# Performance work log

Hardware: AMD Instinct MI355X
Metric: run time of the kernel (lower is better)

The kernel has to match this reference:

```python
import jax, jax.numpy as jnp
import numpy as np

N, E = 50000, 500000
D_IN, D_HID, D_OUT = 512, 512, 256


def setup_inputs() -> dict:
    key = jax.random.key(0)
    ks = jax.random.split(key, 8)
    x = jax.random.normal(ks[0], (N, D_IN), dtype=jnp.float32)
    edge_index1 = jax.random.randint(ks[1], (2, E), 0, N, dtype=jnp.int64)
    edge_index2 = jax.random.randint(ks[2], (2, E), 0, N, dtype=jnp.int64)
    s_in = 1.0 / np.sqrt(D_IN)
    s_hid = 1.0 / np.sqrt(D_HID)
    W1l = jax.random.normal(ks[3], (D_HID, D_IN), dtype=jnp.float32) * s_in
    W1r = jax.random.normal(ks[4], (D_HID, D_IN), dtype=jnp.float32) * s_in
    b1 = jnp.zeros((D_HID,), dtype=jnp.float32)
    W2l = jax.random.normal(ks[5], (D_OUT, D_HID), dtype=jnp.float32) * s_hid
    W2r = jax.random.normal(ks[6], (D_OUT, D_HID), dtype=jnp.float32) * s_hid
    b2 = jnp.zeros((D_OUT,), dtype=jnp.float32)
    return {"x": x, "edge_index1": edge_index1, "edge_index2": edge_index2,
            "W1l": W1l, "b1": b1, "W1r": W1r, "W2l": W2l, "b2": b2, "W2r": W2r}


def _sage_conv(x_src, x_dst, edge_index, Wl, b, Wr):
    # PyG SAGEConv (aggr='mean', root_weight=True): lin_l(mean_agg) + lin_r(x_dst)
    src, dst = edge_index[0], edge_index[1]
    n_dst = x_dst.shape[0]
    msgs = x_src[src]                                        # [E, d] gather
    agg = jax.ops.segment_sum(msgs, dst, num_segments=n_dst)  # [n_dst, d]
    deg = jax.ops.segment_sum(jnp.ones((src.shape[0],), x_src.dtype), dst,
                              num_segments=n_dst)
    agg = agg / jnp.maximum(deg, 1.0)[:, None]                # mean
    return agg @ Wl.T + b + x_dst @ Wr.T


def reference(x, edge_index1, edge_index2, W1l, b1, W1r, W2l, b2, W2r):
    # layer 1 (+ relu; dropout is identity in eval mode)
    h = _sage_conv(x, x, edge_index1, W1l, b1, W1r)
    h = jax.nn.relu(h)
    # layer 2
    h = _sage_conv(h, h, edge_index2, W2l, b2, W2r)
    return jax.nn.log_softmax(h, axis=-1)
```

## Files before the change

kernel.cpp:

```cpp
#include <hip/hip_runtime.h>
#include <math.h>

#define DIN  512
#define DHID 512
#define DOUT 256

typedef __attribute__((ext_vector_type(8))) short short8;
typedef __attribute__((ext_vector_type(4))) float f32x4;
typedef __attribute__((ext_vector_type(2))) float floatx2;

__device__ __forceinline__ unsigned short f2bf(float f) {
    unsigned int u = __float_as_uint(f);
    u += 0x7fffu + ((u >> 16) & 1u);
    return (unsigned short)(u >> 16);
}
__device__ __forceinline__ float bflo(unsigned int w) { return __uint_as_float(w << 16); }
__device__ __forceinline__ float bfhi(unsigned int w) { return __uint_as_float(w & 0xffff0000u); }

__device__ __forceinline__ void cvt8(const float* __restrict__ in,
                                     unsigned short* __restrict__ out, int i) {
    const float4* iv = (const float4*)in;
    float4 a = iv[2 * i], b = iv[2 * i + 1];
    uint4 o;
    o.x = (unsigned)f2bf(a.x) | ((unsigned)f2bf(a.y) << 16);
    o.y = (unsigned)f2bf(a.z) | ((unsigned)f2bf(a.w) << 16);
    o.z = (unsigned)f2bf(b.x) | ((unsigned)f2bf(b.y) << 16);
    o.w = (unsigned)f2bf(b.z) | ((unsigned)f2bf(b.w) << 16);
    ((uint4*)out)[i] = o;
}

__global__ void k_f2bf(const float* __restrict__ in, unsigned short* __restrict__ out, int n8) {
    int i = blockIdx.x * blockDim.x + threadIdx.x;
    if (i < n8) cvt8(in, out, i);
}

__global__ void k_wcvt(const float* __restrict__ W1l, const float* __restrict__ W1r,
                       const float* __restrict__ W2l, const float* __restrict__ W2r,
                       unsigned short* __restrict__ w1, unsigned short* __restrict__ w2) {
    int i = blockIdx.x * blockDim.x + threadIdx.x;
    if (i < 32768)        cvt8(W1l, w1, i);
    else if (i < 65536)   cvt8(W1r, w1 + 262144, i - 32768);
    else if (i < 81920)   cvt8(W2l, w2, i - 65536);
    else if (i < 98304)   cvt8(W2r, w2 + 131072, i - 81920);
}

__global__ void k_count2(const int* __restrict__ d1, const int* __restrict__ d2,
                         int* __restrict__ deg1, int* __restrict__ deg2, int E1, int E2) {
    int e = blockIdx.x * blockDim.x + threadIdx.x;
    if (blockIdx.y == 0) { if (e < E1) atomicAdd(&deg1[d1[e]], 1); }
    else                 { if (e < E2) atomicAdd(&deg2[d2[e]], 1); }
}

#define SCAN_B 256
__global__ void k_scan_partial2(const int* __restrict__ deg1, const int* __restrict__ deg2,
                                int* __restrict__ part1, int* __restrict__ part2, int n) {
    __shared__ int s[SCAN_B];
    const int* deg = blockIdx.y ? deg2 : deg1;
    int* part      = blockIdx.y ? part2 : part1;
    int i = blockIdx.x * SCAN_B + threadIdx.x;
    s[threadIdx.x] = (i < n) ? deg[i] : 0;
    __syncthreads();
    for (int off = SCAN_B / 2; off > 0; off >>= 1) {
        if (threadIdx.x < off) s[threadIdx.x] += s[threadIdx.x + off];
        __syncthreads();
    }
    if (threadIdx.x == 0) part[blockIdx.x] = s[0];
}

__global__ void k_scan_part2b(int* __restrict__ part1, int* __restrict__ part2, int nb,
                              int* __restrict__ rowptr1, int* __restrict__ rowptr2, int n) {
    __shared__ int s[SCAN_B];
    int* part   = blockIdx.x ? part2 : part1;
    int* rowptr = blockIdx.x ? rowptr2 : rowptr1;
    int v = (threadIdx.x < nb) ? part[threadIdx.x] : 0;
    s[threadIdx.x] = v;
    __syncthreads();
    for (int off = 1; off < SCAN_B; off <<= 1) {
        int t = (threadIdx.x >= off) ? s[threadIdx.x - off] : 0;
        __syncthreads();
        s[threadIdx.x] += t;
        __syncthreads();
    }
    if (threadIdx.x < nb) part[threadIdx.x] = s[threadIdx.x] - v;
    if (threadIdx.x == SCAN_B - 1) rowptr[n] = s[SCAN_B - 1];
}

__global__ void k_scan_final2(const int* __restrict__ deg1, const int* __restrict__ deg2,
                              const int* __restrict__ part1, const int* __restrict__ part2,
                              int* __restrict__ rowptr1, int* __restrict__ rowptr2,
                              int* __restrict__ cursor1, int* __restrict__ cursor2, int n) {
    __shared__ int s[SCAN_B];
    const int* deg  = blockIdx.y ? deg2 : deg1;
    const int* part = blockIdx.y ? part2 : part1;
    int* rowptr     = blockIdx.y ? rowptr2 : rowptr1;
    int* cursor     = blockIdx.y ? cursor2 : cursor1;
    int i = blockIdx.x * SCAN_B + threadIdx.x;
    int v = (i < n) ? deg[i] : 0;
    s[threadIdx.x] = v;
    __syncthreads();
    for (int off = 1; off < SCAN_B; off <<= 1) {
        int t = (threadIdx.x >= off) ? s[threadIdx.x - off] : 0;
        __syncthreads();
        s[threadIdx.x] += t;
        __syncthreads();
    }
    if (i < n) {
        int ex = part[blockIdx.y ? blockIdx.x : blockIdx.x] + s[threadIdx.x] - v;
        rowptr[i] = ex;
        cursor[i] = ex;
    }
}

__global__ void k_fill2(const int* __restrict__ s1, const int* __restrict__ d1,
                        const int* __restrict__ s2, const int* __restrict__ d2,
                        int* __restrict__ cur1, int* __restrict__ cur2,
                        int* __restrict__ col1, int* __restrict__ col2, int E1, int E2) {
    int e = blockIdx.x * blockDim.x + threadIdx.x;
    if (blockIdx.y == 0) {
        if (e < E1) { int p = atomicAdd(&cur1[d1[e]], 1); col1[p] = s1[e]; }
    } else {
        if (e < E2) { int p = atomicAdd(&cur2[d2[e]], 1); col2[p] = s2[e]; }
    }
}

#define TM 128
#define TN 128
#define TK 32

template <int NCT, int SPLIT>
__global__ __launch_bounds__(256, 3)
void k_gemm_mfma(const unsigned short* __restrict__ A, const unsigned short* __restrict__ W,
                 unsigned char* __restrict__ C8, unsigned short* __restrict__ C16,
                 int M, int K, int NC) {
    __shared__ __align__(16) unsigned short As[TM * TK];
    __shared__ __align__(16) unsigned short Bs[TN * TK];
    const int id = blockIdx.x;
    const int xcd = id & 7;
    const int s = id >> 3;
    const int row0 = ((s / NCT) * 8 + xcd) * TM;
    const int col0 = (s % NCT) * TN;
    if (row0 >= M) return;

    const int t = threadIdx.x;
    const int lane = t & 63;
    const int w = t >> 6;
    const int wr = (w >> 1) * 64;
    const int wc = (w & 1) * 64;
    const int lm = lane & 15;
    const int k8 = (lane >> 4) * 8;

    f32x4 acc[4][4];
#pragma unroll
    for (int i = 0; i < 4; ++i)
#pragma unroll
        for (int j = 0; j < 4; ++j) acc[i][j] = (f32x4){0.f, 0.f, 0.f, 0.f};

    const int ar = t >> 2;
    const int as = (t & 3) * 8;

    for (int k0 = 0; k0 < K; k0 += TK) {
        int r1 = row0 + ar;      if (r1 >= M) r1 = M - 1;
        int r2 = row0 + ar + 64; if (r2 >= M) r2 = M - 1;
        const unsigned short* ga1 = A + (size_t)r1 * K + k0 + as;
        const unsigned short* ga2 = A + (size_t)r2 * K + k0 + as;
        const unsigned short* gb1 = W + (size_t)(col0 + ar) * K + k0 + as;
        const unsigned short* gb2 = W + (size_t)(col0 + ar + 64) * K + k0 + as;
        __builtin_amdgcn_global_load_lds(
            (const __attribute__((address_space(1))) unsigned int*)ga1,
            (__attribute__((address_space(3))) unsigned int*)&As[t * 8], 16, 0, 0);
        __builtin_amdgcn_global_load_lds(
            (const __attribute__((address_space(1))) unsigned int*)ga2,
            (__attribute__((address_space(3))) unsigned int*)&As[(t + 256) * 8], 16, 0, 0);
        __builtin_amdgcn_global_load_lds(
            (const __attribute__((address_space(1))) unsigned int*)gb1,
            (__attribute__((address_space(3))) unsigned int*)&Bs[t * 8], 16, 0, 0);
        __builtin_amdgcn_global_load_lds(
            (const __attribute__((address_space(1))) unsigned int*)gb2,
            (__attribute__((address_space(3))) unsigned int*)&Bs[(t + 256) * 8], 16, 0, 0);
        __syncthreads();

        short8 a[4], b[4];
#pragma unroll
        for (int i = 0; i < 4; ++i)
            a[i] = *(const short8*)&As[(wr + i * 16 + lm) * TK + k8];
#pragma unroll
        for (int j = 0; j < 4; ++j)
            b[j] = *(const short8*)&Bs[(wc + j * 16 + lm) * TK + k8];
#pragma unroll
        for (int i = 0; i < 4; ++i)
#pragma unroll
            for (int j = 0; j < 4; ++j)
                acc[i][j] = __builtin_amdgcn_mfma_f32_16x16x32_bf16(a[i], b[j], acc[i][j], 0, 0, 0);
        __syncthreads();
    }

    const int qr = (lane >> 4) * 4;
    const bool lo_half = SPLIT && (col0 < NC / 2);
    const int cadj = SPLIT ? NC / 2 : 0;
#pragma unroll
    for (int i = 0; i < 4; ++i) {
#pragma unroll
        for (int r = 0; r < 4; ++r) {
            int gr = row0 + wr + i * 16 + qr + r;
            if (gr >= M) continue;
#pragma unroll
            for (int j = 0; j < 4; ++j) {
                int gc = col0 + wc + j * 16 + lm;
                float v = acc[i][j][r];
                if (SPLIT && lo_half) {
                    int p = __builtin_amdgcn_cvt_pk_fp8_f32(v, v, 0, 0);
                    C8[(size_t)gr * (NC / 2) + gc] = (unsigned char)p;
                } else {
                    C16[(size_t)gr * (NC - cadj) + (gc - cadj)] = f2bf(v);
                }
            }
        }
    }
}

__global__ void k_agg_relu(const unsigned char* __restrict__ C8,
                           const unsigned short* __restrict__ C16r,
                           const int* __restrict__ rowptr, const int* __restrict__ col,
                           const float* __restrict__ b1, unsigned short* __restrict__ H, int n) {
    int node = blockIdx.x * (blockDim.x >> 6) + (threadIdx.x >> 6);
    int lane = threadIdx.x & 63;
    if (node >= n) return;
    int beg = rowptr[node], end = rowptr[node + 1];
    float acc[8] = {};
    const uint2* Cv = (const uint2*)C8;
    int e = beg;
    for (; e + 4 <= end; e += 4) {
        int c0 = col[e], c1 = col[e + 1], c2 = col[e + 2], c3 = col[e + 3];
        uint2 v0 = Cv[(size_t)c0 * 64 + lane];
        uint2 v1 = Cv[(size_t)c1 * 64 + lane];
        uint2 v2 = Cv[(size_t)c2 * 64 + lane];
        uint2 v3 = Cv[(size_t)c3 * 64 + lane];
        unsigned int ws[8] = {v0.x, v0.y, v1.x, v1.y, v2.x, v2.y, v3.x, v3.y};
#pragma unroll
        for (int q = 0; q < 8; ++q) {
            floatx2 flo = __builtin_amdgcn_cvt_pk_f32_fp8(ws[q], 0);
            floatx2 fhi = __builtin_amdgcn_cvt_pk_f32_fp8(ws[q], 1);
            int base = (q & 1) * 4;
            acc[base + 0] += flo.x; acc[base + 1] += flo.y;
            acc[base + 2] += fhi.x; acc[base + 3] += fhi.y;
        }
    }
    for (; e < end; ++e) {
        uint2 v = Cv[(size_t)col[e] * 64 + lane];
        floatx2 f0 = __builtin_amdgcn_cvt_pk_f32_fp8(v.x, 0);
        floatx2 f1 = __builtin_amdgcn_cvt_pk_f32_fp8(v.x, 1);
        floatx2 f2 = __builtin_amdgcn_cvt_pk_f32_fp8(v.y, 0);
        floatx2 f3 = __builtin_amdgcn_cvt_pk_f32_fp8(v.y, 1);
        acc[0] += f0.x; acc[1] += f0.y; acc[2] += f1.x; acc[3] += f1.y;
        acc[4] += f2.x; acc[5] += f2.y; acc[6] += f3.x; acc[7] += f3.y;
    }
    float inv = 1.0f / fmaxf((float)(end - beg), 1.0f);
    uint4 yr = ((const uint4*)C16r)[(size_t)node * 64 + lane];
    unsigned int wr[4] = {yr.x, yr.y, yr.z, yr.w};
    float4 bv0 = ((const float4*)b1)[2 * lane];
    float4 bv1 = ((const float4*)b1)[2 * lane + 1];
    float bb[8] = {bv0.x, bv0.y, bv0.z, bv0.w, bv1.x, bv1.y, bv1.z, bv1.w};
    unsigned int r[4];
#pragma unroll
    for (int q = 0; q < 4; ++q) {
        float v0 = fmaxf(acc[2 * q] * inv     + bflo(wr[q]) + bb[2 * q],     0.f);
        float v1 = fmaxf(acc[2 * q + 1] * inv + bfhi(wr[q]) + bb[2 * q + 1], 0.f);
        r[q] = (unsigned)f2bf(v0) | ((unsigned)f2bf(v1) << 16);
    }
    uint4 o; o.x = r[0]; o.y = r[1]; o.z = r[2]; o.w = r[3];
    ((uint4*)H)[(size_t)node * 64 + lane] = o;
}

__global__ void k_agg_lsm(const unsigned short* __restrict__ C2,
                          const int* __restrict__ rowptr, const int* __restrict__ col,
                          const float* __restrict__ b2, float* __restrict__ O, int n) {
    int node = blockIdx.x * (blockDim.x >> 6) + (threadIdx.x >> 6);
    int lane = threadIdx.x & 63;
    if (node >= n) return;
    int beg = rowptr[node], end = rowptr[node + 1];
    float acc[4] = {};
    const uint2* Cv = (const uint2*)C2;
    int e = beg;
    for (; e + 4 <= end; e += 4) {
        int c0 = col[e], c1 = col[e + 1], c2 = col[e + 2], c3 = col[e + 3];
        uint2 v0 = Cv[(size_t)c0 * 128 + lane];
        uint2 v1 = Cv[(size_t)c1 * 128 + lane];
        uint2 v2 = Cv[(size_t)c2 * 128 + lane];
        uint2 v3 = Cv[(size_t)c3 * 128 + lane];
        acc[0] += bflo(v0.x) + bflo(v1.x) + bflo(v2.x) + bflo(v3.x);
        acc[1] += bfhi(v0.x) + bfhi(v1.x) + bfhi(v2.x) + bfhi(v3.x);
        acc[2] += bflo(v0.y) + bflo(v1.y) + bflo(v2.y) + bflo(v3.y);
        acc[3] += bfhi(v0.y) + bfhi(v1.y) + bfhi(v2.y) + bfhi(v3.y);
    }
    for (; e < end; ++e) {
        uint2 v = Cv[(size_t)col[e] * 128 + lane];
        acc[0] += bflo(v.x); acc[1] += bfhi(v.x);
        acc[2] += bflo(v.y); acc[3] += bfhi(v.y);
    }
    float inv = 1.0f / fmaxf((float)(end - beg), 1.0f);
    uint2 yr = Cv[(size_t)node * 128 + 64 + lane];
    float4 bv = ((const float4*)b2)[lane];
    float val[4];
    val[0] = acc[0] * inv + bflo(yr.x) + bv.x;
    val[1] = acc[1] * inv + bfhi(yr.x) + bv.y;
    val[2] = acc[2] * inv + bflo(yr.y) + bv.z;
    val[3] = acc[3] * inv + bfhi(yr.y) + bv.w;
    float mx = fmaxf(fmaxf(val[0], val[1]), fmaxf(val[2], val[3]));
#pragma unroll
    for (int off = 32; off > 0; off >>= 1) mx = fmaxf(mx, __shfl_xor(mx, off));
    float s = expf(val[0] - mx) + expf(val[1] - mx) + expf(val[2] - mx) + expf(val[3] - mx);
#pragma unroll
    for (int off = 32; off > 0; off >>= 1) s += __shfl_xor(s, off);
    float lse = mx + logf(s);
    float4 o = make_float4(val[0] - lse, val[1] - lse, val[2] - lse, val[3] - lse);
    ((float4*)O)[(size_t)node * 64 + lane] = o;
}

extern "C" void kernel_launch(void* const* d_in, const int* in_sizes, int n_in,
                              void* d_out, int out_size, void* d_ws, size_t ws_size,
                              hipStream_t stream) {
    const float* x   = (const float*)d_in[0];
    const int*   ei1 = (const int*)d_in[1];
    const int*   ei2 = (const int*)d_in[2];
    const float* W1l = (const float*)d_in[3];
    const float* b1  = (const float*)d_in[4];
    const float* W1r = (const float*)d_in[5];
    const float* W2l = (const float*)d_in[6];
    const float* b2  = (const float*)d_in[7];
    const float* W2r = (const float*)d_in[8];
    float* out = (float*)d_out;

    const int N  = in_sizes[0] / DIN;
    const int E1 = in_sizes[1] / 2;
    const int E2 = in_sizes[2] / 2;
    const int Emax = (E1 > E2) ? E1 : E2;
    const int NB = (N + SCAN_B - 1) / SCAN_B;

    unsigned short* x_bf  = (unsigned short*)d_ws;
    unsigned short* h_bf  = x_bf + (size_t)N * 512;
    unsigned char*  c1l   = (unsigned char*)(h_bf + (size_t)N * 512);
    unsigned short* c1r   = (unsigned short*)(c1l + (size_t)N * 512);
    unsigned short* c2    = (unsigned short*)c1l;
    unsigned short* w1_bf = c1r + (size_t)N * 512;
    unsigned short* w2_bf = w1_bf + 1024 * 512;
    int* rowptr1 = (int*)(w2_bf + 512 * 512);
    int* rowptr2 = rowptr1 + (N + 1);
    int* cursor1 = rowptr2 + (N + 1);
    int* cursor2 = cursor1 + N;
    int* deg1    = cursor2 + N;
    int* deg2    = deg1 + N;
    int* part1   = deg2 + N;
    int* part2   = part1 + 256;
    int* col1    = part2 + 256;
    int* col2    = col1 + E1;
    (void)ws_size; (void)n_in; (void)out_size;

    {
        int n8 = N * 512 / 8;
        k_f2bf<<<(n8 + 255) / 256, 256, 0, stream>>>(x, x_bf, n8);
        k_wcvt<<<(98304 + 255) / 256, 256, 0, stream>>>(W1l, W1r, W2l, W2r, w1_bf, w2_bf);
    }

    hipMemsetAsync(deg1, 0, (size_t)2 * N * sizeof(int), stream);
    {
        dim3 ge((Emax + 255) / 256, 2);
        k_count2<<<ge, 256, 0, stream>>>(ei1 + E1, ei2 + E2, deg1, deg2, E1, E2);
        k_scan_partial2<<<dim3(NB, 2), SCAN_B, 0, stream>>>(deg1, deg2, part1, part2, N);
        k_scan_part2b<<<2, SCAN_B, 0, stream>>>(part1, part2, NB, rowptr1, rowptr2, N);
        k_scan_final2<<<dim3(NB, 2), SCAN_B, 0, stream>>>(deg1, deg2, part1, part2,
                                                          rowptr1, rowptr2, cursor1, cursor2, N);
        k_fill2<<<ge, 256, 0, stream>>>(ei1, ei1 + E1, ei2, ei2 + E2,
                                        cursor1, cursor2, col1, col2, E1, E2);
    }

    const int MB = (N + TM - 1) / TM;
    const int G8 = (MB + 7) / 8;

    k_gemm_mfma<8, 1><<<G8 * 8 * 8, 256, 0, stream>>>(x_bf, w1_bf, c1l, c1r, N, DIN, 1024);
    k_agg_relu<<<(N + 3) / 4, 256, 0, stream>>>(c1l, c1r, rowptr1, col1, b1, h_bf, N);

    k_gemm_mfma<4, 0><<<G8 * 8 * 4, 256, 0, stream>>>(h_bf, w2_bf, (unsigned char*)nullptr, c2, N, DHID, 512);
    k_agg_lsm<<<(N + 3) / 4, 256, 0, stream>>>(c2, rowptr2, col2, b2, out, N);
}
```

Before: 504.6 us.

## Swizzle GEMM LDS layout, raise occupancy, store layer-2 neighbor projections as fp8

The GEMM tiles' LDS layout gets an XOR swizzle on the k-chunk index, so the 16-byte fragment reads by MFMA lanes avoid bank conflicts, and launch bounds move from three to four blocks per CU. The second layer's GEMM now uses the split epilogue: the neighbor-projected half is written as fp8 and the root half stays bf16. This halves the bytes gathered per edge in the log-softmax aggregation. The fp8 quantization of layer-2 messages lowers accuracy, and the higher occupancy target may force register spills.

```diff
diff --git a/kernel.cpp b/kernel.cpp
--- a/kernel.cpp
+++ b/kernel.cpp
@@ -105,7 +105,7 @@
         __syncthreads();
     }
     if (i < n) {
-        int ex = part[blockIdx.y ? blockIdx.x : blockIdx.x] + s[threadIdx.x] - v;
+        int ex = part[blockIdx.x] + s[threadIdx.x] - v;
         rowptr[i] = ex;
         cursor[i] = ex;
     }
@@ -128,7 +128,7 @@
 #define TK 32
 
 template <int NCT, int SPLIT>
-__global__ __launch_bounds__(256, 3)
+__global__ __launch_bounds__(256, 4)
 void k_gemm_mfma(const unsigned short* __restrict__ A, const unsigned short* __restrict__ W,
                  unsigned char* __restrict__ C8, unsigned short* __restrict__ C16,
                  int M, int K, int NC) {
@@ -147,7 +147,7 @@
     const int wr = (w >> 1) * 64;
     const int wc = (w & 1) * 64;
     const int lm = lane & 15;
-    const int k8 = (lane >> 4) * 8;
+    const int q = lane >> 4;
 
     f32x4 acc[4][4];
 #pragma unroll
@@ -156,7 +156,7 @@
         for (int j = 0; j < 4; ++j) acc[i][j] = (f32x4){0.f, 0.f, 0.f, 0.f};
 
     const int ar = t >> 2;
-    const int as = (t & 3) * 8;
+    const int as = (((t & 3) ^ ((t >> 3) & 3))) * 8;
 
     for (int k0 = 0; k0 < K; k0 += TK) {
         int r1 = row0 + ar;      if (r1 >= M) r1 = M - 1;
@@ -181,11 +181,15 @@
 
         short8 a[4], b[4];
 #pragma unroll
-        for (int i = 0; i < 4; ++i)
-            a[i] = *(const short8*)&As[(wr + i * 16 + lm) * TK + k8];
-#pragma unroll
-        for (int j = 0; j < 4; ++j)
-            b[j] = *(const short8*)&Bs[(wc + j * 16 + lm) * TK + k8];
+        for (int i = 0; i < 4; ++i) {
+            int R = wr + i * 16 + lm;
+            a[i] = *(const short8*)&As[R * TK + ((q ^ ((R >> 1) & 3)) * 8)];
+        }
+#pragma unroll
+        for (int j = 0; j < 4; ++j) {
+            int R = wc + j * 16 + lm;
+            b[j] = *(const short8*)&Bs[R * TK + ((q ^ ((R >> 1) & 3)) * 8)];
+        }
 #pragma unroll
         for (int i = 0; i < 4; ++i)
 #pragma unroll
@@ -237,10 +241,10 @@
         uint2 v3 = Cv[(size_t)c3 * 64 + lane];
         unsigned int ws[8] = {v0.x, v0.y, v1.x, v1.y, v2.x, v2.y, v3.x, v3.y};
 #pragma unroll
-        for (int q = 0; q < 8; ++q) {
-            floatx2 flo = __builtin_amdgcn_cvt_pk_f32_fp8(ws[q], 0);
-            floatx2 fhi = __builtin_amdgcn_cvt_pk_f32_fp8(ws[q], 1);
-            int base = (q & 1) * 4;
+        for (int qq = 0; qq < 8; ++qq) {
+            floatx2 flo = __builtin_amdgcn_cvt_pk_f32_fp8(ws[qq], 0);
+            floatx2 fhi = __builtin_amdgcn_cvt_pk_f32_fp8(ws[qq], 1);
+            int base = (qq & 1) * 4;
             acc[base + 0] += flo.x; acc[base + 1] += flo.y;
             acc[base + 2] += fhi.x; acc[base + 3] += fhi.y;
         }
@@ -262,16 +266,17 @@
     float bb[8] = {bv0.x, bv0.y, bv0.z, bv0.w, bv1.x, bv1.y, bv1.z, bv1.w};
     unsigned int r[4];
 #pragma unroll
-    for (int q = 0; q < 4; ++q) {
-        float v0 = fmaxf(acc[2 * q] * inv     + bflo(wr[q]) + bb[2 * q],     0.f);
-        float v1 = fmaxf(acc[2 * q + 1] * inv + bfhi(wr[q]) + bb[2 * q + 1], 0.f);
-        r[q] = (unsigned)f2bf(v0) | ((unsigned)f2bf(v1) << 16);
+    for (int qq = 0; qq < 4; ++qq) {
+        float v0 = fmaxf(acc[2 * qq] * inv     + bflo(wr[qq]) + bb[2 * qq],     0.f);
+        float v1 = fmaxf(acc[2 * qq + 1] * inv + bfhi(wr[qq]) + bb[2 * qq + 1], 0.f);
+        r[qq] = (unsigned)f2bf(v0) | ((unsigned)f2bf(v1) << 16);
     }
     uint4 o; o.x = r[0]; o.y = r[1]; o.z = r[2]; o.w = r[3];
     ((uint4*)H)[(size_t)node * 64 + lane] = o;
 }
 
-__global__ void k_agg_lsm(const unsigned short* __restrict__ C2,
+__global__ void k_agg_lsm(const unsigned char* __restrict__ C8,
+                          const unsigned short* __restrict__ C16r,
                           const int* __restrict__ rowptr, const int* __restrict__ col,
                           const float* __restrict__ b2, float* __restrict__ O, int n) {
     int node = blockIdx.x * (blockDim.x >> 6) + (threadIdx.x >> 6);
@@ -279,26 +284,30 @@
     if (node >= n) return;
     int beg = rowptr[node], end = rowptr[node + 1];
     float acc[4] = {};
-    const uint2* Cv = (const uint2*)C2;
+    const unsigned int* Cv = (const unsigned int*)C8;
     int e = beg;
     for (; e + 4 <= end; e += 4) {
         int c0 = col[e], c1 = col[e + 1], c2 = col[e + 2], c3 = col[e + 3];
-        uint2 v0 = Cv[(size_t)c0 * 128 + lane];
-        uint2 v1 = Cv[(size_t)c1 * 128 + lane];
-        uint2 v2 = Cv[(size_t)c2 * 128 + lane];
-        uint2 v3 = Cv[(size_t)c3 * 128 + lane];
-        acc[0] += bflo(v0.x) + bflo(v1.x) + bflo(v2.x) + bflo(v3.x);
-        acc[1] += bfhi(v0.x) + bfhi(v1.x) + bfhi(v2.x) + bfhi(v3.x);
-        acc[2] += bflo(v0.y) + bflo(v1.y) + bflo(v2.y) + bflo(v3.y);
-        acc[3] += bfhi(v0.y) + bfhi(v1.y) + bfhi(v2.y) + bfhi(v3.y);
+        unsigned int u0 = Cv[(size_t)c0 * 64 + lane];
+        unsigned int u1 = Cv[(size_t)c1 * 64 + lane];
+        unsigned int u2 = Cv[(size_t)c2 * 64 + lane];
+        unsigned int u3 = Cv[(size_t)c3 * 64 + lane];
+        unsigned int us[4] = {u0, u1, u2, u3};
+#pragma unroll
+        for (int qq = 0; qq < 4; ++qq) {
+            floatx2 flo = __builtin_amdgcn_cvt_pk_f32_fp8(us[qq], 0);
+            floatx2 fhi = __builtin_amdgcn_cvt_pk_f32_fp8(us[qq], 1);
+            acc[0] += flo.x; acc[1] += flo.y; acc[2] += fhi.x; acc[3] += fhi.y;
+        }
     }
     for (; e < end; ++e) {
-        uint2 v = Cv[(size_t)col[e] * 128 + lane];
-        acc[0] += bflo(v.x); acc[1] += bfhi(v.x);
-        acc[2] += bflo(v.y); acc[3] += bfhi(v.y);
+        unsigned int u = Cv[(size_t)col[e] * 64 + lane];
+        floatx2 flo = __builtin_amdgcn_cvt_pk_f32_fp8(u, 0);
+        floatx2 fhi = __builtin_amdgcn_cvt_pk_f32_fp8(u, 1);
+        acc[0] += flo.x; acc[1] += flo.y; acc[2] += fhi.x; acc[3] += fhi.y;
     }
     float inv = 1.0f / fmaxf((float)(end - beg), 1.0f);
-    uint2 yr = Cv[(size_t)node * 128 + 64 + lane];
+    uint2 yr = ((const uint2*)C16r)[(size_t)node * 64 + lane];
     float4 bv = ((const float4*)b2)[lane];
     float val[4];
     val[0] = acc[0] * inv + bflo(yr.x) + bv.x;
@@ -340,7 +349,8 @@
     unsigned short* h_bf  = x_bf + (size_t)N * 512;
     unsigned char*  c1l   = (unsigned char*)(h_bf + (size_t)N * 512);
     unsigned short* c1r   = (unsigned short*)(c1l + (size_t)N * 512);
-    unsigned short* c2    = (unsigned short*)c1l;
+    unsigned char*  c2l   = c1l;
+    unsigned short* c2r   = (unsigned short*)(c2l + (size_t)N * 256);
     unsigned short* w1_bf = c1r + (size_t)N * 512;
     unsigned short* w2_bf = w1_bf + 1024 * 512;
     int* rowptr1 = (int*)(w2_bf + 512 * 512);
@@ -379,6 +389,6 @@
     k_gemm_mfma<8, 1><<<G8 * 8 * 8, 256, 0, stream>>>(x_bf, w1_bf, c1l, c1r, N, DIN, 1024);
     k_agg_relu<<<(N + 3) / 4, 256, 0, stream>>>(c1l, c1r, rowptr1, col1, b1, h_bf, N);
 
-    k_gemm_mfma<4, 0><<<G8 * 8 * 4, 256, 0, stream>>>(h_bf, w2_bf, (unsigned char*)nullptr, c2, N, DHID, 512);
-    k_agg_lsm<<<(N + 3) / 4, 256, 0, stream>>>(c2, rowptr2, col2, b2, out, N);
-}
+    k_gemm_mfma<4, 1><<<G8 * 8 * 4, 256, 0, stream>>>(h_bf, w2_bf, c2l, c2r, N, DHID, 512);
+    k_agg_lsm<<<(N + 3) / 4, 256, 0, stream>>>(c2l, c2r, rowptr2, col2, b2, out, N);
+}
```

Measured after the change: 500.4 us. About the same (-0.8%).
